# Kernel optimization log

Measured on AMD Instinct MI355X. Metric: run time of the kernel, lower is better.

The kernel has to match this reference:

```python
import jax, jax.numpy as jnp
import numpy as np
import math

B, L, D, K = 16, 8192, 256, 320
BN_EPS = 1e-5


def setup_inputs() -> dict:
    key = jax.random.key(0)
    k1, k2, k3, k4 = jax.random.split(key, 4)
    x = jax.random.normal(k1, (B, L, D), dtype=jnp.float32)
    bn_weight = 1.0 + 0.1 * jax.random.normal(k2, (D,), dtype=jnp.float32)
    bn_bias = 0.1 * jax.random.normal(k3, (D,), dtype=jnp.float32)
    # xavier_uniform for Embedding(numCodes, codeDim)
    a = math.sqrt(6.0 / (K + D))
    codebook = jax.random.uniform(k4, (K, D), minval=-a, maxval=a, dtype=jnp.float32)
    return {"x": x, "bn_weight": bn_weight, "bn_bias": bn_bias, "codebook": codebook}


def batchnorm1d(x, weight, bias):
    # BatchNorm1d in training mode: stats over (batch, length) per channel,
    # biased variance for normalization (matches torch).
    mean = jnp.mean(x, axis=(0, 1))
    var = jnp.var(x, axis=(0, 1))
    return (x - mean) * jax.lax.rsqrt(var + BN_EPS) * weight + bias


def reference(x, bn_weight, bn_bias, codebook):
    xb = batchnorm1d(x, bn_weight, bn_bias)            # [B, L, D]
    flat = xb.reshape(-1, D)                           # [B*L, D]
    # squared euclidean distance (same argmin as torch.cdist)
    d2 = (jnp.sum(flat * flat, axis=-1, keepdims=True)
          - 2.0 * flat @ codebook.T
          + jnp.sum(codebook * codebook, axis=-1))     # [B*L, K]
    indices = jnp.argmin(d2, axis=-1)                  # [B*L]
    codes = codebook[indices].reshape(B, L, D)         # gather nearest codes
    return codes, indices.reshape(B, L, 1)
```

## Files before the change

kernel.cpp:

```cpp
#include <hip/hip_runtime.h>
#include <hip/hip_bf16.h>

#define NROW 131072
#define D 256
#define K 320
#define BN_EPS 1e-5f
#define FIXSCALE 16777216.0f

typedef _Float16 half8 __attribute__((ext_vector_type(8)));
typedef float f32x4 __attribute__((ext_vector_type(4)));


__global__ __launch_bounds__(256) void k_stats_partial(const float* __restrict__ x,
                                                       unsigned long long* __restrict__ acc) {
  const int d = threadIdx.x;
  const int blk = blockIdx.x;
  const float* p = x + (size_t)blk * 256 * D + d;
  float s = 0.f, q = 0.f;
  #pragma unroll 4
  for (int r = 0; r < 256; ++r) {
    float v = p[(size_t)r * D];
    s += v;
    q = fmaf(v, v, q);
  }
  long long si = llrintf(s * FIXSCALE);
  long long qi = llrintf(q * FIXSCALE);
  atomicAdd(&acc[d],       (unsigned long long)si);
  atomicAdd(&acc[256 + d], (unsigned long long)qi);
}

__global__ __launch_bounds__(256) void k_stats_final(const unsigned long long* __restrict__ acc,
                                                     const float* __restrict__ cb,
                                                     float* __restrict__ meanb,
                                                     float* __restrict__ rsb,
                                                     float* __restrict__ cnorm) {
  const int t = threadIdx.x;
  if (blockIdx.x == 0) {
    double s = (double)(long long)acc[t]       / (double)FIXSCALE;
    double q = (double)(long long)acc[256 + t] / (double)FIXSCALE;
    double mean = s / (double)NROW;
    double var  = q / (double)NROW - mean * mean;
    meanb[t] = (float)mean;
    rsb[t]   = (float)(1.0 / sqrt(var + (double)BN_EPS));
  } else {
    for (int code = t; code < K; code += 256) {
      const float* c = cb + (size_t)code * D;
      float s = 0.f;
      for (int dd = 0; dd < D; ++dd) s = fmaf(c[dd], c[dd], s);
      cnorm[code] = s;
    }
  }
}

__global__ __launch_bounds__(64) void k_cbprep(const float* __restrict__ cb,
                                               _Float16* __restrict__ cbx,
                                               unsigned long long* __restrict__ acc) {
  const int b = blockIdx.x;
  const int l = threadIdx.x;
  if (b == 160) {
    #pragma unroll
    for (int j = 0; j < 8; ++j) acc[j * 64 + l] = 0ull;
    return;
  }
  const int nt = b >> 3;
  const int ks = b & 7;
  const int code = nt * 16 + (l & 15);
  const int d0 = ks * 32 + (l >> 4) * 8;
  const float* src = cb + (size_t)code * D + d0;
  const size_t bh = ((size_t)(nt * 2 + 0) * 8 + ks) * 512 + l * 8;
  const size_t bl = ((size_t)(nt * 2 + 1) * 8 + ks) * 512 + l * 8;
  #pragma unroll
  for (int j = 0; j < 8; ++j) {
    float v = src[j];
    _Float16 h = (_Float16)v;
    _Float16 lo = (_Float16)(v - (float)h);
    cbx[bh + j] = h;
    cbx[bl + j] = lo;
  }
}

__global__ __launch_bounds__(256) void k_main(const float* __restrict__ x,
                                              const float* __restrict__ w,
                                              const float* __restrict__ bias,
                                              const float* __restrict__ cb,
                                              const float* __restrict__ meanb,
                                              const float* __restrict__ rsb,
                                              const float* __restrict__ cnorm,
                                              const _Float16* __restrict__ cbx,
                                              float* __restrict__ out) {
  __shared__ _Float16 Bbuf[2][8192];
  __shared__ float sxs[128];
  __shared__ int bsel[128];

  const int t = threadIdx.x;
  const int lane = t & 63;
  const int wv = t >> 6;
  const int c15 = lane & 15;
  const int g = lane >> 4;
  const int row0 = (int)blockIdx.x * 128;

  float4 s0, s1, s2, s3;
  const char* stg_src = (const char*)cbx + (size_t)t * 16;
#define ISSUE(c) {                                                  \
    const char* p_ = stg_src + (size_t)(c) * 16384;                 \
    s0 = *(const float4*)(p_);                                      \
    s1 = *(const float4*)(p_ + 4096);                               \
    s2 = *(const float4*)(p_ + 8192);                               \
    s3 = *(const float4*)(p_ + 12288);                              \
  }
#define WRITE(b) {                                                  \
    char* q_ = (char*)Bbuf[(b)] + t * 16;                           \
    *(float4*)(q_)         = s0;                                    \
    *(float4*)(q_ + 4096)  = s1;                                    \
    *(float4*)(q_ + 8192)  = s2;                                    \
    *(float4*)(q_ + 12288) = s3;                                    \
  }

  ISSUE(0);

  half8 ah[2][8], al[2][8];
  float accq0 = 0.f, accq1 = 0.f;
  {
    const int dbase = g * 8;
    const float* xp0 = x + (size_t)(row0 + wv * 32 + c15) * D + dbase;
    const float* xp1 = x + (size_t)(row0 + wv * 32 + 16 + c15) * D + dbase;
    #pragma unroll
    for (int ks = 0; ks < 8; ++ks) {
      const int d0 = dbase + ks * 32;
      float4 m0 = *(const float4*)(meanb + d0);
      float4 m1 = *(const float4*)(meanb + d0 + 4);
      float4 r0 = *(const float4*)(rsb + d0);
      float4 r1 = *(const float4*)(rsb + d0 + 4);
      float4 w0 = *(const float4*)(w + d0);
      float4 w1 = *(const float4*)(w + d0 + 4);
      float4 b0 = *(const float4*)(bias + d0);
      float4 b1 = *(const float4*)(bias + d0 + 4);
      {
        float4 xa = *(const float4*)(xp0 + ks * 32);
        float4 xb2 = *(const float4*)(xp0 + ks * 32 + 4);
        float o0 = ((xa.x - m0.x) * r0.x) * w0.x + b0.x;
        float o1 = ((xa.y - m0.y) * r0.y) * w0.y + b0.y;
        float o2 = ((xa.z - m0.z) * r0.z) * w0.z + b0.z;
        float o3 = ((xa.w - m0.w) * r0.w) * w0.w + b0.w;
        float o4 = ((xb2.x - m1.x) * r1.x) * w1.x + b1.x;
        float o5 = ((xb2.y - m1.y) * r1.y) * w1.y + b1.y;
        float o6 = ((xb2.z - m1.z) * r1.z) * w1.z + b1.z;
        float o7 = ((xb2.w - m1.w) * r1.w) * w1.w + b1.w;
        accq0 = fmaf(o0, o0, accq0); accq0 = fmaf(o1, o1, accq0);
        accq0 = fmaf(o2, o2, accq0); accq0 = fmaf(o3, o3, accq0);
        accq0 = fmaf(o4, o4, accq0); accq0 = fmaf(o5, o5, accq0);
        accq0 = fmaf(o6, o6, accq0); accq0 = fmaf(o7, o7, accq0);
        _Float16 h;
        h = (_Float16)o0; ah[0][ks][0] = h; al[0][ks][0] = (_Float16)(o0 - (float)h);
        h = (_Float16)o1; ah[0][ks][1] = h; al[0][ks][1] = (_Float16)(o1 - (float)h);
        h = (_Float16)o2; ah[0][ks][2] = h; al[0][ks][2] = (_Float16)(o2 - (float)h);
        h = (_Float16)o3; ah[0][ks][3] = h; al[0][ks][3] = (_Float16)(o3 - (float)h);
        h = (_Float16)o4; ah[0][ks][4] = h; al[0][ks][4] = (_Float16)(o4 - (float)h);
        h = (_Float16)o5; ah[0][ks][5] = h; al[0][ks][5] = (_Float16)(o5 - (float)h);
        h = (_Float16)o6; ah[0][ks][6] = h; al[0][ks][6] = (_Float16)(o6 - (float)h);
        h = (_Float16)o7; ah[0][ks][7] = h; al[0][ks][7] = (_Float16)(o7 - (float)h);
      }
      {
        float4 xa = *(const float4*)(xp1 + ks * 32);
        float4 xb2 = *(const float4*)(xp1 + ks * 32 + 4);
        float o0 = ((xa.x - m0.x) * r0.x) * w0.x + b0.x;
        float o1 = ((xa.y - m0.y) * r0.y) * w0.y + b0.y;
        float o2 = ((xa.z - m0.z) * r0.z) * w0.z + b0.z;
        float o3 = ((xa.w - m0.w) * r0.w) * w0.w + b0.w;
        float o4 = ((xb2.x - m1.x) * r1.x) * w1.x + b1.x;
        float o5 = ((xb2.y - m1.y) * r1.y) * w1.y + b1.y;
        float o6 = ((xb2.z - m1.z) * r1.z) * w1.z + b1.z;
        float o7 = ((xb2.w - m1.w) * r1.w) * w1.w + b1.w;
        accq1 = fmaf(o0, o0, accq1); accq1 = fmaf(o1, o1, accq1);
        accq1 = fmaf(o2, o2, accq1); accq1 = fmaf(o3, o3, accq1);
        accq1 = fmaf(o4, o4, accq1); accq1 = fmaf(o5, o5, accq1);
        accq1 = fmaf(o6, o6, accq1); accq1 = fmaf(o7, o7, accq1);
        _Float16 h;
        h = (_Float16)o0; ah[1][ks][0] = h; al[1][ks][0] = (_Float16)(o0 - (float)h);
        h = (_Float16)o1; ah[1][ks][1] = h; al[1][ks][1] = (_Float16)(o1 - (float)h);
        h = (_Float16)o2; ah[1][ks][2] = h; al[1][ks][2] = (_Float16)(o2 - (float)h);
        h = (_Float16)o3; ah[1][ks][3] = h; al[1][ks][3] = (_Float16)(o3 - (float)h);
        h = (_Float16)o4; ah[1][ks][4] = h; al[1][ks][4] = (_Float16)(o4 - (float)h);
        h = (_Float16)o5; ah[1][ks][5] = h; al[1][ks][5] = (_Float16)(o5 - (float)h);
        h = (_Float16)o6; ah[1][ks][6] = h; al[1][ks][6] = (_Float16)(o6 - (float)h);
        h = (_Float16)o7; ah[1][ks][7] = h; al[1][ks][7] = (_Float16)(o7 - (float)h);
      }
    }
  }

  WRITE(0);
  ISSUE(1);

  {
    float v0 = accq0 + __shfl_xor(accq0, 16);
    float sx0 = v0 + __shfl_xor(v0, 32);
    float v1 = accq1 + __shfl_xor(accq1, 16);
    float sx1 = v1 + __shfl_xor(v1, 32);
    if (lane < 16) {
      sxs[wv * 32 + lane]      = sx0;
      sxs[wv * 32 + 16 + lane] = sx1;
    }
  }
  __syncthreads();

  float bv[2][4];
  int   bix[2][4];
  #pragma unroll
  for (int i = 0; i < 2; ++i)
    #pragma unroll
    for (int r = 0; r < 4; ++r) { bv[i][r] = 3.4e38f; bix[i][r] = 0x7fffffff; }

  float sxr[2][4];
  #pragma unroll
  for (int i = 0; i < 2; ++i)
    #pragma unroll
    for (int r = 0; r < 4; ++r) sxr[i][r] = sxs[wv * 32 + i * 16 + g * 4 + r];

  for (int c = 0; c < 20; ++c) {
    if (c + 1 < 20) WRITE((c + 1) & 1);
    if (c + 2 < 20) ISSUE(c + 2);

    {
      const _Float16* bb = Bbuf[c & 1] + lane * 8;
      f32x4 acc0 = (f32x4){0.f, 0.f, 0.f, 0.f};
      f32x4 acc1 = (f32x4){0.f, 0.f, 0.f, 0.f};
      #pragma unroll
      for (int ks = 0; ks < 8; ++ks) {
        half8 bh = *(const half8*)(bb + ks * 512);
        half8 bl = *(const half8*)(bb + 4096 + ks * 512);
        acc0 = __builtin_amdgcn_mfma_f32_16x16x32_f16(ah[0][ks], bh, acc0, 0, 0, 0);
        acc0 = __builtin_amdgcn_mfma_f32_16x16x32_f16(ah[0][ks], bl, acc0, 0, 0, 0);
        acc0 = __builtin_amdgcn_mfma_f32_16x16x32_f16(al[0][ks], bh, acc0, 0, 0, 0);
        acc1 = __builtin_amdgcn_mfma_f32_16x16x32_f16(ah[1][ks], bh, acc1, 0, 0, 0);
        acc1 = __builtin_amdgcn_mfma_f32_16x16x32_f16(ah[1][ks], bl, acc1, 0, 0, 0);
        acc1 = __builtin_amdgcn_mfma_f32_16x16x32_f16(al[1][ks], bh, acc1, 0, 0, 0);
      }
      const int code = c * 16 + c15;
      const float cn = cnorm[code];
      #pragma unroll
      for (int r = 0; r < 4; ++r) {
        const float d20 = (sxr[0][r] - 2.0f * acc0[r]) + cn;
        if (d20 < bv[0][r] || (d20 == bv[0][r] && code < bix[0][r])) {
          bv[0][r] = d20; bix[0][r] = code;
        }
        const float d21 = (sxr[1][r] - 2.0f * acc1[r]) + cn;
        if (d21 < bv[1][r] || (d21 == bv[1][r] && code < bix[1][r])) {
          bv[1][r] = d21; bix[1][r] = code;
        }
      }
    }
    if (c < 19) __syncthreads();
  }

  #pragma unroll
  for (int off = 8; off >= 1; off >>= 1) {
    #pragma unroll
    for (int i = 0; i < 2; ++i)
      #pragma unroll
      for (int r = 0; r < 4; ++r) {
        const float ov = __shfl_xor(bv[i][r], off);
        const int   oi = __shfl_xor(bix[i][r], off);
        if (ov < bv[i][r] || (ov == bv[i][r] && oi < bix[i][r])) {
          bv[i][r] = ov; bix[i][r] = oi;
        }
      }
  }
  if (c15 == 0) {
    #pragma unroll
    for (int i = 0; i < 2; ++i)
      #pragma unroll
      for (int r = 0; r < 4; ++r) {
        const int row = wv * 32 + i * 16 + g * 4 + r;
        bsel[row] = bix[i][r];
        out[(size_t)NROW * D + row0 + row] = (float)bix[i][r];
      }
  }
  __syncthreads();

  {
    const int lr = t >> 1;
    const int q = t & 1;
    const int code = bsel[lr];
    const float* cp = cb + (size_t)code * D;
    float* op = out + (size_t)(row0 + lr) * D;
    #pragma unroll
    for (int e = 0; e < 32; ++e) {
      *(float4*)(op + (e * 2 + q) * 4) = *(const float4*)(cp + (e * 2 + q) * 4);
    }
  }
#undef ISSUE
#undef WRITE
}

extern "C" void kernel_launch(void* const* d_in, const int* in_sizes, int n_in,
                              void* d_out, int out_size, void* d_ws, size_t ws_size,
                              hipStream_t stream) {
  const float* x    = (const float*)d_in[0];
  const float* w    = (const float*)d_in[1];
  const float* bias = (const float*)d_in[2];
  const float* cb   = (const float*)d_in[3];
  float* out = (float*)d_out;

  unsigned long long* acc = (unsigned long long*)d_ws;
  float* meanb = (float*)((char*)d_ws + 4096);
  float* rsb   = meanb + 256;
  float* cnorm = rsb + 256;
  _Float16* cbx = (_Float16*)((char*)d_ws + 8192);

  k_cbprep<<<161, 64, 0, stream>>>(cb, cbx, acc);
  k_stats_partial<<<512, 256, 0, stream>>>(x, acc);
  k_stats_final<<<2, 256, 0, stream>>>(acc, cb, meanb, rsb, cnorm);
  k_main<<<NROW / 128, 256, 0, stream>>>(x, w, bias, cb, meanb, rsb, cnorm, cbx, out);
}
```

Before: 165.7 us.

## Double k_main block to 512 threads and vectorize stats partial reduction

k_main now uses 512 threads and processes 256 rows per block, so each staged codebook chunk in shared memory is shared by twice as many waves and each thread issues half the staging loads. The stats partial kernel reads float4 per thread and has each wave cover one 256-row slab, which cuts the block count and does one atomic per channel per slab. The larger block may lower occupancy or raise register pressure, and the sxs/bsel sizing assumes the hidden body indexes consistently with 8 waves.

After: 209.9 us. +26.7%, slower.

```diff
diff --git a/kernel.cpp b/kernel.cpp
--- a/kernel.cpp
+++ b/kernel.cpp
@@ -13,20 +13,28 @@
 
 __global__ __launch_bounds__(256) void k_stats_partial(const float* __restrict__ x,
                                                        unsigned long long* __restrict__ acc) {
-  const int d = threadIdx.x;
-  const int blk = blockIdx.x;
-  const float* p = x + (size_t)blk * 256 * D + d;
-  float s = 0.f, q = 0.f;
+  const int q = threadIdx.x & 63;
+  const int g2 = threadIdx.x >> 6;
+  const int slab = (int)blockIdx.x * 4 + g2;
+  const float* p = x + (size_t)slab * 256 * D + q * 4;
+  float s0 = 0.f, s1 = 0.f, s2 = 0.f, s3 = 0.f;
+  float q0 = 0.f, q1 = 0.f, q2 = 0.f, q3 = 0.f;
   #pragma unroll 4
   for (int r = 0; r < 256; ++r) {
-    float v = p[(size_t)r * D];
-    s += v;
-    q = fmaf(v, v, q);
-  }
-  long long si = llrintf(s * FIXSCALE);
-  long long qi = llrintf(q * FIXSCALE);
-  atomicAdd(&acc[d],       (unsigned long long)si);
-  atomicAdd(&acc[256 + d], (unsigned long long)qi);
+    float4 v = *(const float4*)(p + (size_t)r * D);
+    s0 += v.x; q0 = fmaf(v.x, v.x, q0);
+    s1 += v.y; q1 = fmaf(v.y, v.y, q1);
+    s2 += v.z; q2 = fmaf(v.z, v.z, q2);
+    s3 += v.w; q3 = fmaf(v.w, v.w, q3);
+  }
+  atomicAdd(&acc[q * 4 + 0],       (unsigned long long)(long long)llrintf(s0 * FIXSCALE));
+  atomicAdd(&acc[q * 4 + 1],       (unsigned long long)(long long)llrintf(s1 * FIXSCALE));
+  atomicAdd(&acc[q * 4 + 2],       (unsigned long long)(long long)llrintf(s2 * FIXSCALE));
+  atomicAdd(&acc[q * 4 + 3],       (unsigned long long)(long long)llrintf(s3 * FIXSCALE));
+  atomicAdd(&acc[256 + q * 4 + 0], (unsigned long long)(long long)llrintf(q0 * FIXSCALE));
+  atomicAdd(&acc[256 + q * 4 + 1], (unsigned long long)(long long)llrintf(q1 * FIXSCALE));
+  atomicAdd(&acc[256 + q * 4 + 2], (unsigned long long)(long long)llrintf(q2 * FIXSCALE));
+  atomicAdd(&acc[256 + q * 4 + 3], (unsigned long long)(long long)llrintf(q3 * FIXSCALE));
 }
 
 __global__ __launch_bounds__(256) void k_stats_final(const unsigned long long* __restrict__ acc,
@@ -79,7 +87,7 @@
   }
 }
 
-__global__ __launch_bounds__(256) void k_main(const float* __restrict__ x,
+__global__ __launch_bounds__(512) void k_main(const float* __restrict__ x,
                                               const float* __restrict__ w,
                                               const float* __restrict__ bias,
                                               const float* __restrict__ cb,
@@ -89,31 +97,27 @@
                                               const _Float16* __restrict__ cbx,
                                               float* __restrict__ out) {
   __shared__ _Float16 Bbuf[2][8192];
-  __shared__ float sxs[128];
-  __shared__ int bsel[128];
+  __shared__ float sxs[256];
+  __shared__ int bsel[256];
 
   const int t = threadIdx.x;
   const int lane = t & 63;
   const int wv = t >> 6;
   const int c15 = lane & 15;
   const int g = lane >> 4;
-  const int row0 = (int)blockIdx.x * 128;
-
-  float4 s0, s1, s2, s3;
+  const int row0 = (int)blockIdx.x * 256;
+
+  float4 s0, s1;
   const char* stg_src = (const char*)cbx + (size_t)t * 16;
 #define ISSUE(c) {                                                  \
     const char* p_ = stg_src + (size_t)(c) * 16384;                 \
     s0 = *(const float4*)(p_);                                      \
-    s1 = *(const float4*)(p_ + 4096);                               \
-    s2 = *(const float4*)(p_ + 8192);                               \
-    s3 = *(const float4*)(p_ + 12288);                              \
+    s1 = *(const float4*)(p_ + 8192);                               \
   }
 #define WRITE(b) {                                                  \
     char* q_ = (char*)Bbuf[(b)] + t * 16;                           \
-    *(float4*)(q_)         = s0;                                    \
-    *(float4*)(q_ + 4096)  = s1;                                    \
-    *(float4*)(q_ + 8192)  = s2;                                    \
-    *(float4*)(q_ + 12288) = s3;                                    \
+    *(float4*)(q_)        = s0;                                     \
+    *(float4*)(q_ + 8192) = s1;                                     \
   }
 
   ISSUE(0);
@@ -308,7 +312,7 @@
   _Float16* cbx = (_Float16*)((char*)d_ws + 8192);
 
   k_cbprep<<<161, 64, 0, stream>>>(cb, cbx, acc);
-  k_stats_partial<<<512, 256, 0, stream>>>(x, acc);
+  k_stats_partial<<<128, 256, 0, stream>>>(x, acc);
   k_stats_final<<<2, 256, 0, stream>>>(acc, cb, meanb, rsb, cnorm);
-  k_main<<<NROW / 128, 256, 0, stream>>>(x, w, bias, cb, meanb, rsb, cnorm, cbx, out);
-}
+  k_main<<<NROW / 256, 512, 0, stream>>>(x, w, bias, cb, meanb, rsb, cnorm, cbx, out);
+}
```
